# Kernel optimization log

Measured on AMD Instinct MI355X. Metric: run time of the kernel, lower is better.

The kernel has to match this reference:

```python
import jax, jax.numpy as jnp
import numpy as np

B, NZ, ND, SDIM, H = 16384, 64, 8, 128, 512


def setup_inputs() -> dict:
    key = jax.random.key(0)
    ks = jax.random.split(key, 20)
    n = lambda i, shape, scale=0.02: (jax.random.normal(ks[i], shape, jnp.float32) * scale)
    return {
        "z": jax.random.normal(ks[0], (B, NZ), jnp.float32),
        "y": jax.random.randint(ks[1], (B,), 0, ND),
        # shared MLP: nz->512, 512->512 x3, ReLU after each
        "W0": n(2, (NZ, H)), "b0": jnp.zeros((H,), jnp.float32),
        "W1": n(3, (H, H)),  "b1": jnp.zeros((H,), jnp.float32),
        "W2": n(4, (H, H)),  "b2": jnp.zeros((H,), jnp.float32),
        "W3": n(5, (H, H)),  "b3": jnp.zeros((H,), jnp.float32),
        "U1": n(6, (ND, H, H)), "c1": jnp.zeros((ND, 1, H), jnp.float32),
        "U2": n(7, (ND, H, H)), "c2": jnp.zeros((ND, 1, H), jnp.float32),
        "U3": n(8, (ND, H, H)), "c3": jnp.zeros((ND, 1, H), jnp.float32),
        "Uo": n(9, (ND, H, SDIM)), "co": jnp.zeros((ND, 1, SDIM), jnp.float32),
    }


def reference(z, y, W0, b0, W1, b1, W2, b2, W3, b3, U1, c1, U2, c2, U3, c3, Uo, co):
    # shared trunk: [B, nz] -> [B, 512]
    h = jax.nn.relu(z @ W0 + b0)
    h = jax.nn.relu(h @ W1 + b1)
    h = jax.nn.relu(h @ W2 + b2)
    h = jax.nn.relu(h @ W3 + b3)
    # densely compute all nd unshared branches (faithful to torch stack-then-index)
    s = jax.nn.relu(jnp.einsum('bh,dhk->dbk', h, U1) + c1)   # [nd, B, 512]
    s = jax.nn.relu(jnp.einsum('dbh,dhk->dbk', s, U2) + c2)
    s = jax.nn.relu(jnp.einsum('dbh,dhk->dbk', s, U3) + c3)
    s = jnp.einsum('dbh,dhk->dbk', s, Uo) + co               # [nd, B, sdim]
    # gather-select the branch indexed by each sample's domain label y
    return s[y, jnp.arange(z.shape[0])]                      # [B, sdim]
```

## Files before the change

### kernel.cpp

```cpp
#include <hip/hip_runtime.h>

#define B_    16384
#define NZ_   64
#define ND_   8
#define SDIM_ 128
#define H_    512
#define CAP_  2320
#define NTB_  29

typedef _Float16 f16;
typedef __attribute__((ext_vector_type(4))) _Float16 half4;
typedef __attribute__((ext_vector_type(8))) _Float16 half8;
typedef __attribute__((ext_vector_type(4))) float floatx4;

#define VMCNT4 asm volatile("s_waitcnt vmcnt(4)" ::: "memory")
#define VMCNT1 asm volatile("s_waitcnt vmcnt(1)" ::: "memory")
#define VMCNT0 asm volatile("s_waitcnt vmcnt(0)" ::: "memory")
#define LGKM0  asm volatile("s_waitcnt lgkmcnt(0)" ::: "memory")

__device__ __forceinline__ void gload16(const void* gp, void* lp) {
    void* g = const_cast<void*>(gp);
    __builtin_amdgcn_global_load_lds(
        (__attribute__((address_space(1))) void*)g,
        (__attribute__((address_space(3))) void*)lp, 16, 0, 0);
}

__device__ __forceinline__ int pswz_t(int row, int colbyte) {
    return (row * 1024 + colbyte) ^ (((row >> 1) & 7) << 4);
}
__device__ __forceinline__ int pswz_b(int row, int colbyte) {
    return (row * 1024 + colbyte) ^ ((row & 7) << 4);
}

__device__ __forceinline__ void tr_mat(float (*tb)[33], const float* __restrict__ s,
                                       f16* __restrict__ dd, int K, int N, int tl) {
    const int ntk = K >> 5;
    const int per = ntk * (N >> 5);
    const int bt  = tl / per;
    const int w   = tl - bt * per;
    s  += (size_t)bt * K * N;
    dd += (size_t)bt * K * N;
    const int k0 = (w % ntk) << 5, n0 = (w / ntk) << 5;
    const int tid = threadIdx.x;
    {
        const int nn = tid & 31, k4 = tid >> 5;
        #pragma unroll
        for (int p = 0; p < 4; p++)
            tb[k4 + p * 8][nn] = s[(size_t)(k0 + k4 + p * 8) * N + n0 + nn];
    }
    __syncthreads();
    {
        const int sub = tid >> 7, r = tid & 127;
        const int lane = r >> 1, jp = (r & 1) * 4;
        const int kb = lane >> 4, l15 = lane & 15;
        const size_t base = ((size_t)((n0 >> 4) + sub) * (K >> 5) + (k0 >> 5)) * 512
                          + lane * 8 + jp;
        half4 h;
        #pragma unroll
        for (int jj = 0; jj < 4; jj++)
            h[jj] = (f16)tb[kb * 8 + jp + jj][sub * 16 + l15];
        *(half4*)(dd + base) = h;
    }
}

__global__ __launch_bounds__(256) void tr_k(
    const float* W0, const float* W1, const float* W2, const float* W3,
    const float* U1, const float* U2, const float* U3, const float* Uo,
    f16* W0t, f16* W1t, f16* W2t, f16* W3t,
    f16* U1t, f16* U2t, f16* U3t, f16* Uot)
{
    __shared__ float tb[32][33];
    int tl = blockIdx.x;
    if (tl < 32)   { tr_mat(tb, W0, W0t, 64, 512, tl); return; }  tl -= 32;
    if (tl < 256)  { tr_mat(tb, W1, W1t, 512, 512, tl); return; } tl -= 256;
    if (tl < 256)  { tr_mat(tb, W2, W2t, 512, 512, tl); return; } tl -= 256;
    if (tl < 256)  { tr_mat(tb, W3, W3t, 512, 512, tl); return; } tl -= 256;
    if (tl < 2048) { tr_mat(tb, U1, U1t, 512, 512, tl); return; } tl -= 2048;
    if (tl < 2048) { tr_mat(tb, U2, U2t, 512, 512, tl); return; } tl -= 2048;
    if (tl < 2048) { tr_mat(tb, U3, U3t, 512, 512, tl); return; } tl -= 2048;
    tr_mat(tb, Uo, Uot, 512, 128, tl);
}
#define TR_BLOCKS 7456

__global__ __launch_bounds__(256) void sort_k(const int* __restrict__ y,
                                              int* __restrict__ cnt,
                                              int* __restrict__ rowmap) {
    __shared__ int h[ND_], base[ND_];
    if (threadIdx.x < ND_) h[threadIdx.x] = 0;
    __syncthreads();
    const int b = blockIdx.x * 256 + threadIdx.x;
    const int d = y[b];
    const int r = atomicAdd(&h[d], 1);
    __syncthreads();
    if (threadIdx.x < ND_) base[threadIdx.x] = atomicAdd(&cnt[threadIdx.x], h[threadIdx.x]);
    __syncthreads();
    rowmap[d * CAP_ + base[d] + r] = b;
}

template<int MFRAG, int NFRAG, int KT, int NFN, int KTN, int SB, bool RELU, bool TOPANEL>
__device__ __forceinline__ void layer_t(
    char* lds, const half8* __restrict__ wp, const half8* __restrict__ wpn,
    const float* __restrict__ bias, half8 (&b)[3][4])
{
    const int t = threadIdx.x;
    const int lane = t & 63, wid = t >> 6;
    const int l15 = lane & 15, kb = lane >> 4;

    int baseA[MFRAG];
    #pragma unroll
    for (int m = 0; m < MFRAG; m++)
        baseA[m] = (((m * 16 + l15) * 1024) + kb * 16) ^ (((l15 >> 1) & 7) << 4);

    half8 a[2][MFRAG];
    #pragma unroll
    for (int m = 0; m < MFRAG; m++) a[0][m] = *(const half8*)(lds + baseA[m]);

    floatx4 acc[MFRAG][NFRAG] = {};

    #pragma unroll
    for (int kt = 0; kt < KT; kt++) {
        const int cur = kt & 1;
        if (kt + 1 < KT) {
            #pragma unroll
            for (int m = 0; m < MFRAG; m++)
                a[cur ^ 1][m] = *(const half8*)(lds + (baseA[m] ^ ((kt + 1) << 6)));
        }
        if (kt + 2 < KT) {
            #pragma unroll
            for (int n = 0; n < NFRAG; n++)
                b[(SB + kt + 2) % 3][n] = wp[((wid * NFRAG + n) * KT + kt + 2) * 64 + lane];
        } else if constexpr (NFN > 0) {
            const int s2 = kt + 2 - KT;
            #pragma unroll
            for (int n = 0; n < NFN; n++)
                b[(SB + kt + 2) % 3][n] = wpn[((wid * NFN + n) * KTN + s2) * 64 + lane];
        }
        __builtin_amdgcn_s_setprio(1);
        #pragma unroll
        for (int m = 0; m < MFRAG; m++)
            #pragma unroll
            for (int n = 0; n < NFRAG; n++)
                acc[m][n] = __builtin_amdgcn_mfma_f32_16x16x32_f16(
                    a[cur][m], b[(SB + kt) % 3][n], acc[m][n], 0, 0, 0);
        __builtin_amdgcn_s_setprio(0);
    }

    __syncthreads();

    #pragma unroll
    for (int n = 0; n < NFRAG; n++) {
        const int col = wid * (NFRAG * 16) + n * 16 + l15;
        const float bb = bias[col];
        #pragma unroll
        for (int m = 0; m < MFRAG; m++) {
            #pragma unroll
            for (int e = 0; e < 4; e++) {
                const int row = m * 16 + kb * 4 + e;
                float v = acc[m][n][e] + bb;
                if constexpr (RELU) v = fmaxf(v, 0.0f);
                *(f16*)(lds + pswz_t(row, col * 2)) = (f16)v;
            }
        }
    }
    __syncthreads();
}

__global__ __launch_bounds__(512, 2) void trunk_k(
    const float* __restrict__ z,
    const f16* __restrict__ W0p, const float* __restrict__ b0,
    const f16* __restrict__ W1p, const float* __restrict__ b1,
    const f16* __restrict__ W2p, const float* __restrict__ b2,
    const f16* __restrict__ W3p, const float* __restrict__ b3,
    f16* __restrict__ hT)
{
    extern __shared__ char lds[];
    const int t = threadIdx.x;
    const int row0 = blockIdx.x * 64;
    const int lane = t & 63, wid = t >> 6;

    const half8* w0 = (const half8*)W0p;
    const half8* w1 = (const half8*)W1p;
    const half8* w2 = (const half8*)W2p;
    const half8* w3 = (const half8*)W3p;

    half8 b[3][4];
    #pragma unroll
    for (int s = 0; s < 2; s++)
        #pragma unroll
        for (int n = 0; n < 4; n++)
            b[s][n] = w0[((wid * 4 + n) * 2 + s) * 64 + lane];

    {
        const int r = t >> 3, c = (t & 7) * 8;
        const float4 v0 = *(const float4*)(z + (size_t)(row0 + r) * NZ_ + c);
        const float4 v1 = *(const float4*)(z + (size_t)(row0 + r) * NZ_ + c + 4);
        half8 h = { (f16)v0.x, (f16)v0.y, (f16)v0.z, (f16)v0.w,
                    (f16)v1.x, (f16)v1.y, (f16)v1.z, (f16)v1.w };
        *(half8*)(lds + pswz_t(r, c * 2)) = h;
    }
    __syncthreads();

    layer_t<4, 4, 2,  4, 16, 0, true, true>(lds, w0, w1, b0, b);
    layer_t<4, 4, 16, 4, 16, 2, true, true>(lds, w1, w2, b1, b);
    layer_t<4, 4, 16, 4, 16, 0, true, true>(lds, w2, w3, b2, b);
    layer_t<4, 4, 16, 0, 16, 1, true, true>(lds, w3, w3, b3, b);

    {
        const int r = t >> 3;
        #pragma unroll
        for (int p = 0; p < 8; p++) {
            const int c16 = (t & 7) + p * 8;
            half8 h = *(const half8*)(lds + pswz_t(r, c16 * 16));
            *(half8*)(hT + (size_t)(row0 + r) * H_ + c16 * 8) = h;
        }
    }
}

template<int MFRAG, int NFRAG, int KT, bool RELU, bool TOPANEL>
__device__ __forceinline__ void layer_c(
    char* lds, char* ldsB, const f16* __restrict__ Wp, const float* __restrict__ bias,
    float* __restrict__ outf, const int* __restrict__ rmt, int vend)
{
    const int t = threadIdx.x;
    const int lane = t & 63, wid = t >> 6;
    const int l15 = lane & 15, kb = lane >> 4;
    const int swz = (l15 & 7) << 4;
    constexpr int BUFSZ = 8 * NFRAG * 1024;

    int baseA[MFRAG];
    #pragma unroll
    for (int m = 0; m < MFRAG; m++)
        baseA[m] = (((m * 16 + l15) * 1024) + kb * 16) ^ swz;

    char* chunk = ldsB + wid * (NFRAG * 1024);
    const f16* gw = Wp + (size_t)wid * NFRAG * KT * 512 + lane * 8;

    auto stage = [&](int s) {
        #pragma unroll
        for (int n = 0; n < NFRAG; n++)
            gload16(gw + ((size_t)n * KT + s) * 512,
                    chunk + (s & 1) * BUFSZ + n * 1024);
    };
    auto readB = [&](int s, half8 (&br)[NFRAG]) {
        #pragma unroll
        for (int n = 0; n < NFRAG; n++)
            br[n] = *(const half8*)(chunk + (s & 1) * BUFSZ + n * 1024 + lane * 16);
    };

    half8 a[2][MFRAG], br[2][NFRAG];
    floatx4 acc[MFRAG][NFRAG] = {};

    stage(0); stage(1);
    if constexpr (NFRAG == 4) VMCNT4; else VMCNT1;
    readB(0, br[0]);
    #pragma unroll
    for (int m = 0; m < MFRAG; m++) a[0][m] = *(const half8*)(lds + baseA[m]);

    #pragma unroll
    for (int kt = 0; kt < KT; kt++) {
        const int cur = kt & 1, nxt = cur ^ 1;
        __builtin_amdgcn_s_setprio(1);
        #pragma unroll
        for (int m = 0; m < MFRAG; m++)
            #pragma unroll
            for (int n = 0; n < NFRAG; n++)
                acc[m][n] = __builtin_amdgcn_mfma_f32_16x16x32_f16(
                    a[cur][m], br[cur][n], acc[m][n], 0, 0, 0);
        __builtin_amdgcn_s_setprio(0);
        if (kt + 2 < KT) {
            LGKM0;
            stage(kt + 2);
        }
        if (kt + 1 < KT) {
            if (kt + 2 < KT) { if constexpr (NFRAG == 4) VMCNT4; else VMCNT1; }
            else             { VMCNT0; }
            readB(kt + 1, br[nxt]);
            #pragma unroll
            for (int m = 0; m < MFRAG; m++)
                a[nxt][m] = *(const half8*)(lds + (baseA[m] ^ ((kt + 1) << 6)));
        }
    }

    __syncthreads();

    #pragma unroll
    for (int n = 0; n < NFRAG; n++) {
        const int col = wid * (NFRAG * 16) + n * 16 + l15;
        const float bb = bias[col];
        #pragma unroll
        for (int m = 0; m < MFRAG; m++) {
            #pragma unroll
            for (int e = 0; e < 4; e++) {
                const int row = m * 16 + kb * 4 + e;
                float v = acc[m][n][e] + bb;
                if constexpr (RELU) v = fmaxf(v, 0.0f);
                if constexpr (TOPANEL) {
                    *(f16*)(lds + pswz_b(row, col * 2)) = (f16)v;
                } else {
                    if (row < vend) outf[(size_t)rmt[row] * SDIM_ + col] = v;
                }
            }
        }
    }
    if constexpr (TOPANEL) __syncthreads();
}

__global__ __launch_bounds__(512, 1) void branch_k(
    const f16* __restrict__ hT,
    const f16* __restrict__ U1p, const float* __restrict__ c1,
    const f16* __restrict__ U2p, const float* __restrict__ c2,
    const f16* __restrict__ U3p, const float* __restrict__ c3,
    const f16* __restrict__ Uop, const float* __restrict__ co,
    const int* __restrict__ cnt, const int* __restrict__ rowmap,
    float* __restrict__ out)
{
    extern __shared__ char lds[];
    char* ldsB = lds + 80 * 1024;
    const int d = blockIdx.x & 7, i = blockIdx.x >> 3;
    const int c = cnt[d];
    if (i * 80 >= c) return;
    const int vend = c - i * 80;
    const int* rmt = rowmap + d * CAP_ + i * 80;
    const int t = threadIdx.x;

    #pragma unroll
    for (int p = 0; p < 10; p++) {
        const int r   = p * 8 + (t >> 6);
        const int c16 = t & 63;
        const int src = rmt[r];
        half8 h = *(const half8*)(hT + (size_t)src * H_ + c16 * 8);
        *(half8*)(lds + pswz_b(r, c16 * 16)) = h;
    }
    __syncthreads();

    const f16* u1 = U1p + (size_t)d * H_ * H_;
    const f16* u2 = U2p + (size_t)d * H_ * H_;
    const f16* u3 = U3p + (size_t)d * H_ * H_;
    const f16* uo = Uop + (size_t)d * H_ * SDIM_;

    layer_c<5, 4, 16, true,  true >(lds, ldsB, u1, c1 + d * H_,    nullptr, nullptr, 0);
    layer_c<5, 4, 16, true,  true >(lds, ldsB, u2, c2 + d * H_,    nullptr, nullptr, 0);
    layer_c<5, 4, 16, true,  true >(lds, ldsB, u3, c3 + d * H_,    nullptr, nullptr, 0);
    layer_c<5, 1, 16, false, false>(lds, ldsB, uo, co + d * SDIM_, out, rmt, vend);
}

extern "C" void kernel_launch(void* const* d_in, const int* in_sizes, int n_in,
                              void* d_out, int out_size, void* d_ws, size_t ws_size,
                              hipStream_t stream)
{
    const float* z  = (const float*)d_in[0];
    const int*   y  = (const int*)d_in[1];
    const float* W0 = (const float*)d_in[2];
    const float* b0 = (const float*)d_in[3];
    const float* W1 = (const float*)d_in[4];
    const float* b1 = (const float*)d_in[5];
    const float* W2 = (const float*)d_in[6];
    const float* b2 = (const float*)d_in[7];
    const float* W3 = (const float*)d_in[8];
    const float* b3 = (const float*)d_in[9];
    const float* U1 = (const float*)d_in[10];
    const float* c1 = (const float*)d_in[11];
    const float* U2 = (const float*)d_in[12];
    const float* c2 = (const float*)d_in[13];
    const float* U3 = (const float*)d_in[14];
    const float* c3 = (const float*)d_in[15];
    const float* Uo = (const float*)d_in[16];
    const float* co = (const float*)d_in[17];
    float* out = (float*)d_out;

    char* p = (char*)d_ws;
    auto take = [&](size_t nbytes) { char* r = p; p += (nbytes + 255) & ~(size_t)255; return r; };
    int* cnt    = (int*)take(ND_ * 4);
    int* rowmap = (int*)take((size_t)ND_ * CAP_ * 4);
    f16* W0t = (f16*)take((size_t)H_ * NZ_ * 2);
    f16* W1t = (f16*)take((size_t)H_ * H_ * 2);
    f16* W2t = (f16*)take((size_t)H_ * H_ * 2);
    f16* W3t = (f16*)take((size_t)H_ * H_ * 2);
    f16* U1t = (f16*)take((size_t)ND_ * H_ * H_ * 2);
    f16* U2t = (f16*)take((size_t)ND_ * H_ * H_ * 2);
    f16* U3t = (f16*)take((size_t)ND_ * H_ * H_ * 2);
    f16* Uot = (f16*)take((size_t)ND_ * SDIM_ * H_ * 2);
    f16* hT  = (f16*)take((size_t)B_ * H_ * 2);

    hipFuncSetAttribute((const void*)trunk_k,  hipFuncAttributeMaxDynamicSharedMemorySize, 64 * 1024);
    hipFuncSetAttribute((const void*)branch_k, hipFuncAttributeMaxDynamicSharedMemorySize, 144 * 1024);

    hipMemsetAsync(cnt, 0, ND_ * 4, stream);
    hipMemsetAsync(rowmap, 0, (size_t)ND_ * CAP_ * 4, stream);
    sort_k<<<dim3(B_ / 256), dim3(256), 0, stream>>>(y, cnt, rowmap);

    tr_k<<<dim3(TR_BLOCKS), dim3(256), 0, stream>>>(W0, W1, W2, W3, U1, U2, U3, Uo,
                                                    W0t, W1t, W2t, W3t, U1t, U2t, U3t, Uot);

    trunk_k<<<dim3(B_ / 64), dim3(512), 64 * 1024, stream>>>(
        z, W0t, b0, W1t, b1, W2t, b2, W3t, b3, hT);

    branch_k<<<dim3(8 * NTB_), dim3(512), 144 * 1024, stream>>>(
        hT, U1t, c1, U2t, c2, U3t, c3, Uot, co, cnt, rowmap, out);
}
```

Baseline: 89.64 us.

## Fuse sort, branch weight transpose and trunk MLP into one heterogeneous kernel

Trunk-weight transposes move into a small separate kernel. The branch-weight transpose and the domain sort now run inside the trunk kernel as extra block roles, so that work overlaps with the trunk MLP and fewer kernels are launched. The rowmap memset is removed; tail rows are clamped to the last valid row instead. Nontemporal load and store hints are added for hT reads and output writes. This can unbalance block scheduling, and the launch-bounds occupancy hint of 2 is dropped for the trunk.

New measurement: 88.64 us. Within noise of the previous version (-1.1%).

```diff
diff --git a/kernel.cpp b/kernel.cpp
--- a/kernel.cpp
+++ b/kernel.cpp
@@ -33,7 +33,8 @@
 }
 
 __device__ __forceinline__ void tr_mat(float (*tb)[33], const float* __restrict__ s,
-                                       f16* __restrict__ dd, int K, int N, int tl) {
+                                       f16* __restrict__ dd, int K, int N, int tl,
+                                       int tid) {
     const int ntk = K >> 5;
     const int per = ntk * (N >> 5);
     const int bt  = tl / per;
@@ -41,7 +42,6 @@
     s  += (size_t)bt * K * N;
     dd += (size_t)bt * K * N;
     const int k0 = (w % ntk) << 5, n0 = (w / ntk) << 5;
-    const int tid = threadIdx.x;
     {
         const int nn = tid & 31, k4 = tid >> 5;
         #pragma unroll
@@ -63,41 +63,19 @@
     }
 }
 
-__global__ __launch_bounds__(256) void tr_k(
+__global__ __launch_bounds__(256) void tr_w_k(
     const float* W0, const float* W1, const float* W2, const float* W3,
-    const float* U1, const float* U2, const float* U3, const float* Uo,
-    f16* W0t, f16* W1t, f16* W2t, f16* W3t,
-    f16* U1t, f16* U2t, f16* U3t, f16* Uot)
+    f16* W0t, f16* W1t, f16* W2t, f16* W3t)
 {
     __shared__ float tb[32][33];
     int tl = blockIdx.x;
-    if (tl < 32)   { tr_mat(tb, W0, W0t, 64, 512, tl); return; }  tl -= 32;
-    if (tl < 256)  { tr_mat(tb, W1, W1t, 512, 512, tl); return; } tl -= 256;
-    if (tl < 256)  { tr_mat(tb, W2, W2t, 512, 512, tl); return; } tl -= 256;
-    if (tl < 256)  { tr_mat(tb, W3, W3t, 512, 512, tl); return; } tl -= 256;
-    if (tl < 2048) { tr_mat(tb, U1, U1t, 512, 512, tl); return; } tl -= 2048;
-    if (tl < 2048) { tr_mat(tb, U2, U2t, 512, 512, tl); return; } tl -= 2048;
-    if (tl < 2048) { tr_mat(tb, U3, U3t, 512, 512, tl); return; } tl -= 2048;
-    tr_mat(tb, Uo, Uot, 512, 128, tl);
-}
-#define TR_BLOCKS 7456
-
-__global__ __launch_bounds__(256) void sort_k(const int* __restrict__ y,
-                                              int* __restrict__ cnt,
-                                              int* __restrict__ rowmap) {
-    __shared__ int h[ND_], base[ND_];
-    if (threadIdx.x < ND_) h[threadIdx.x] = 0;
-    __syncthreads();
-    const int b = blockIdx.x * 256 + threadIdx.x;
-    const int d = y[b];
-    const int r = atomicAdd(&h[d], 1);
-    __syncthreads();
-    if (threadIdx.x < ND_) base[threadIdx.x] = atomicAdd(&cnt[threadIdx.x], h[threadIdx.x]);
-    __syncthreads();
-    rowmap[d * CAP_ + base[d] + r] = b;
-}
-
-template<int MFRAG, int NFRAG, int KT, int NFN, int KTN, int SB, bool RELU, bool TOPANEL>
+    if (tl < 32)   { tr_mat(tb, W0, W0t, 64, 512, tl, threadIdx.x); return; }  tl -= 32;
+    if (tl < 256)  { tr_mat(tb, W1, W1t, 512, 512, tl, threadIdx.x); return; } tl -= 256;
+    if (tl < 256)  { tr_mat(tb, W2, W2t, 512, 512, tl, threadIdx.x); return; } tl -= 256;
+    tr_mat(tb, W3, W3t, 512, 512, tl, threadIdx.x);
+}
+
+template<int MFRAG, int NFRAG, int KT, int NFN, int KTN, int SB, bool RELU>
 __device__ __forceinline__ void layer_t(
     char* lds, const half8* __restrict__ wp, const half8* __restrict__ wpn,
     const float* __restrict__ bias, half8 (&b)[3][4])
@@ -165,17 +143,52 @@
     __syncthreads();
 }
 
-__global__ __launch_bounds__(512, 2) void trunk_k(
+__global__ __launch_bounds__(512) void mega_k(
     const float* __restrict__ z,
     const f16* __restrict__ W0p, const float* __restrict__ b0,
     const f16* __restrict__ W1p, const float* __restrict__ b1,
     const f16* __restrict__ W2p, const float* __restrict__ b2,
     const f16* __restrict__ W3p, const float* __restrict__ b3,
-    f16* __restrict__ hT)
+    f16* __restrict__ hT,
+    const float* U1, const float* U2, const float* U3, const float* Uo,
+    f16* U1t, f16* U2t, f16* U3t, f16* Uot,
+    const int* __restrict__ y, int* __restrict__ cnt, int* __restrict__ rowmap)
 {
     extern __shared__ char lds[];
+    const int bid = blockIdx.x;
     const int t = threadIdx.x;
-    const int row0 = blockIdx.x * 64;
+
+    if (bid >= 512) {
+        int* h    = (int*)lds;
+        int* basep = h + 8;
+        if (t < ND_) h[t] = 0;
+        __syncthreads();
+        const int b = (bid - 512) * 512 + t;
+        const int d = y[b];
+        const int r = atomicAdd(&h[d], 1);
+        __syncthreads();
+        if (t < ND_) basep[t] = atomicAdd(&cnt[t], h[t]);
+        __syncthreads();
+        rowmap[d * CAP_ + basep[d] + r] = b;
+        return;
+    }
+
+    if (bid >= 256) {
+        const int sub = t >> 8;
+        const int tid = t & 255;
+        float (*tb)[33] = (float(*)[33])(lds + sub * 4352);
+        for (int pp = bid - 256; pp < 3328; pp += 256) {
+            int tl = pp * 2 + sub;
+            if (tl < 2048)      tr_mat(tb, U1, U1t, 512, 512, tl, tid);
+            else if (tl < 4096) tr_mat(tb, U2, U2t, 512, 512, tl - 2048, tid);
+            else if (tl < 6144) tr_mat(tb, U3, U3t, 512, 512, tl - 4096, tid);
+            else                tr_mat(tb, Uo, Uot, 512, 128, tl - 6144, tid);
+            __syncthreads();
+        }
+        return;
+    }
+
+    const int row0 = bid * 64;
     const int lane = t & 63, wid = t >> 6;
 
     const half8* w0 = (const half8*)W0p;
@@ -200,10 +213,10 @@
     }
     __syncthreads();
 
-    layer_t<4, 4, 2,  4, 16, 0, true, true>(lds, w0, w1, b0, b);
-    layer_t<4, 4, 16, 4, 16, 2, true, true>(lds, w1, w2, b1, b);
-    layer_t<4, 4, 16, 4, 16, 0, true, true>(lds, w2, w3, b2, b);
-    layer_t<4, 4, 16, 0, 16, 1, true, true>(lds, w3, w3, b3, b);
+    layer_t<4, 4, 2,  4, 16, 0, true>(lds, w0, w1, b0, b);
+    layer_t<4, 4, 16, 4, 16, 2, true>(lds, w1, w2, b1, b);
+    layer_t<4, 4, 16, 4, 16, 0, true>(lds, w2, w3, b2, b);
+    layer_t<4, 4, 16, 0, 16, 1, true>(lds, w3, w3, b3, b);
 
     {
         const int r = t >> 3;
@@ -297,7 +310,8 @@
                 if constexpr (TOPANEL) {
                     *(f16*)(lds + pswz_b(row, col * 2)) = (f16)v;
                 } else {
-                    if (row < vend) outf[(size_t)rmt[row] * SDIM_ + col] = v;
+                    if (row < vend)
+                        __builtin_nontemporal_store(v, &outf[(size_t)rmt[row] * SDIM_ + col]);
                 }
             }
         }
@@ -326,9 +340,10 @@
     #pragma unroll
     for (int p = 0; p < 10; p++) {
         const int r   = p * 8 + (t >> 6);
+        const int rr  = (r < vend) ? r : (vend - 1);
         const int c16 = t & 63;
-        const int src = rmt[r];
-        half8 h = *(const half8*)(hT + (size_t)src * H_ + c16 * 8);
+        const int src = rmt[rr];
+        half8 h = __builtin_nontemporal_load((const half8*)(hT + (size_t)src * H_ + c16 * 8));
         *(half8*)(lds + pswz_b(r, c16 * 16)) = h;
     }
     __syncthreads();
@@ -382,18 +397,17 @@
     f16* Uot = (f16*)take((size_t)ND_ * SDIM_ * H_ * 2);
     f16* hT  = (f16*)take((size_t)B_ * H_ * 2);
 
-    hipFuncSetAttribute((const void*)trunk_k,  hipFuncAttributeMaxDynamicSharedMemorySize, 64 * 1024);
+    hipFuncSetAttribute((const void*)mega_k,   hipFuncAttributeMaxDynamicSharedMemorySize, 64 * 1024);
     hipFuncSetAttribute((const void*)branch_k, hipFuncAttributeMaxDynamicSharedMemorySize, 144 * 1024);
 
     hipMemsetAsync(cnt, 0, ND_ * 4, stream);
-    hipMemsetAsync(rowmap, 0, (size_t)ND_ * CAP_ * 4, stream);
-    sort_k<<<dim3(B_ / 256), dim3(256), 0, stream>>>(y, cnt, rowmap);
-
-    tr_k<<<dim3(TR_BLOCKS), dim3(256), 0, stream>>>(W0, W1, W2, W3, U1, U2, U3, Uo,
-                                                    W0t, W1t, W2t, W3t, U1t, U2t, U3t, Uot);
-
-    trunk_k<<<dim3(B_ / 64), dim3(512), 64 * 1024, stream>>>(
-        z, W0t, b0, W1t, b1, W2t, b2, W3t, b3, hT);
+
+    tr_w_k<<<dim3(800), dim3(256), 0, stream>>>(W0, W1, W2, W3, W0t, W1t, W2t, W3t);
+
+    mega_k<<<dim3(544), dim3(512), 64 * 1024, stream>>>(
+        z, W0t, b0, W1t, b1, W2t, b2, W3t, b3, hT,
+        U1, U2, U3, Uo, U1t, U2t, U3t, Uot,
+        y, cnt, rowmap);
 
     branch_k<<<dim3(8 * NTB_), dim3(512), 144 * 1024, stream>>>(
         hT, U1t, c1, U2t, c2, U3t, c3, Uot, co, cnt, rowmap, out);
```
